# Kernel tuning notes

Measured on AMD Instinct MI355X. Metric: run time of the kernel, lower is better.

## Reference

```python
import jax, jax.numpy as jnp
import numpy as np

B, N_ROWS, N_COLS, CTRL = 16384, 2048, 128, 1024
EPS = 1e-16


def setup_inputs() -> dict:
    key = jax.random.key(0)
    k1, k2, k3 = jax.random.split(key, 3)
    x = jax.random.normal(k1, (B, CTRL), dtype=jnp.float32)
    W_fc = jax.random.normal(k2, (CTRL, N_COLS + 6), dtype=jnp.float32) * 0.02
    b_fc = jnp.zeros((N_COLS + 6,), dtype=jnp.float32)
    M = jax.random.normal(k3, (N_ROWS, N_COLS), dtype=jnp.float32)
    # initial weighting: softmax of bias with w_bias[0]=100 -> ~one-hot at row 0
    w_bias = jnp.zeros((N_ROWS,), dtype=jnp.float32).at[0].set(100.0)
    w_prev = jnp.broadcast_to(jax.nn.softmax(w_bias), (B, N_ROWS))
    return {"x": x, "W_fc": W_fc, "b_fc": b_fc, "M": M, "w_prev": w_prev}


def reference(x, W_fc, b_fc, M, w_prev):
    # dense projection + split
    h = x @ W_fc + b_fc                      # [B, N_COLS+6]
    k = h[:, :N_COLS]                        # [B, N_COLS]
    beta = jax.nn.softplus(h[:, N_COLS:N_COLS + 1])          # [B, 1]
    g = jax.nn.sigmoid(h[:, N_COLS + 1:N_COLS + 2])          # [B, 1]
    s = jax.nn.softmax(h[:, N_COLS + 2:N_COLS + 5], axis=-1) # [B, 3]
    gamma = 1.0 + jax.nn.softplus(h[:, N_COLS + 5:N_COLS + 6])  # [B, 1]

    # content addressing: cosine similarity against every memory row
    k_norm = jnp.linalg.norm(k, axis=-1, keepdims=True)       # [B, 1]
    M_norm = jnp.linalg.norm(M, axis=-1)                      # [N_ROWS]
    sim = (k @ M.T) / (k_norm * M_norm[None, :] + EPS)        # [B, N_ROWS]
    w_c = jax.nn.softmax(beta * sim, axis=-1)

    # interpolation gate
    w_g = g * w_c + (1.0 - g) * w_prev

    # circular shift convolution (shifts -1, 0, +1)
    w_tilde = (s[:, 0:1] * jnp.roll(w_g, 1, axis=1)
               + s[:, 1:2] * w_g
               + s[:, 2:3] * jnp.roll(w_g, -1, axis=1))

    # sharpening
    w_pow = (w_tilde + EPS) ** gamma
    w = w_pow / jnp.sum(w_pow, axis=-1, keepdims=True)

    # weighted read
    r = w @ M                                                 # [B, N_COLS]
    return r
```

## Files before the change

### kernel.cpp

```cpp
#include <hip/hip_runtime.h>
#include <hip/hip_bf16.h>

#define NB    16384
#define NR    2048
#define NC    128
#define KCTRL 1024
#define EPSF  1e-16f
#define ESTR  2056
#define XSTR  1032

typedef __attribute__((ext_vector_type(8))) short bf16x8;
typedef __attribute__((ext_vector_type(4))) float f32x4;

__device__ __forceinline__ float softplus_f(float x) {
    return fmaxf(x, 0.f) + log1pf(__expf(-fabsf(x)));
}
__device__ __forceinline__ unsigned short f2bf(float f) {
    __hip_bfloat16 h = __float2bfloat16(f);
    return *(unsigned short*)&h;
}
__device__ __forceinline__ float bf2f(unsigned short u) {
    __hip_bfloat16 h;
    *(unsigned short*)&h = u;
    return __bfloat162float(h);
}

__device__ __forceinline__ size_t swz(int n, int k, int nch) {
    return ((size_t)((n >> 4) * nch + (k >> 5)) * 64 + ((k >> 3) & 3) * 16 + (n & 15)) * 8 + (k & 7);
}

__global__ __launch_bounds__(64) void prep_all(const float* __restrict__ M,
                                               unsigned short* __restrict__ Mb_sw,
                                               unsigned short* __restrict__ Mt_sw,
                                               float* __restrict__ imn,
                                               const float* __restrict__ W,
                                               unsigned short* __restrict__ Wt_sw) {
    const int bid = blockIdx.x;
    const int l = threadIdx.x;
    if (bid < NR) {
        const int i = bid;
        const float v0 = M[(size_t)i * NC + l];
        const float v1 = M[(size_t)i * NC + 64 + l];
        Mb_sw[swz(i, l, 4)]      = f2bf(v0);
        Mb_sw[swz(i, 64 + l, 4)] = f2bf(v1);
        Mt_sw[swz(l, i, 64)]      = f2bf(v0);
        Mt_sw[swz(64 + l, i, 64)] = f2bf(v1);
        float s = v0 * v0 + v1 * v1;
        #pragma unroll
        for (int m = 1; m < 64; m <<= 1) s += __shfl_xor(s, m);
        if (l == 0) imn[i] = 1.f / sqrtf(s);
    } else {
        const int k = bid - NR;
        Wt_sw[swz(l, k, 32)]      = f2bf(W[(size_t)k * 134 + l]);
        Wt_sw[swz(64 + l, k, 32)] = f2bf(W[(size_t)k * 134 + 64 + l]);
        if (l < 6) {
            Wt_sw[swz(128 + l, k, 32)] = f2bf(W[(size_t)k * 134 + 128 + l]);
        }
    }
}

__global__ __launch_bounds__(512, 4) void fused_ntm(const float* __restrict__ x,
                                                    const unsigned short* __restrict__ Wt_sw,
                                                    const float* __restrict__ bfc,
                                                    const unsigned short* __restrict__ Mb_sw,
                                                    const unsigned short* __restrict__ Mt_sw,
                                                    const float* __restrict__ imn,
                                                    const float* __restrict__ wprev,
                                                    float* __restrict__ out) {
    __shared__ __align__(16) unsigned short E_s[16][ESTR];
    __shared__ __align__(16) unsigned short k_s[16][136];
    __shared__ float h6s[16][6];
    __shared__ float ksum[16];
    __shared__ float scal_s[16][6];
    __shared__ float wred[16][8];
    __shared__ float fa_s[16], fc_s[16], invZ_s[16];

    unsigned short (*x_s)[XSTR] = (unsigned short(*)[XSTR])E_s;

    const int tid  = threadIdx.x;
    const int w    = tid >> 6;
    const int lane = tid & 63;
    const int quad = lane >> 4;
    const int l16  = lane & 15;
    const int b0   = blockIdx.x * 16;

    if (tid < 16) ksum[tid] = 0.f;

    #pragma unroll
    for (int p = 0; p < 8; p++) {
        const int idx = p * 512 + tid;
        const int row = idx >> 8;
        const int c4  = idx & 255;
        const float4 v = *(const float4*)(x + (size_t)(b0 + row) * KCTRL + c4 * 4);
        unsigned short* d = &x_s[row][c4 * 4];
        d[0] = f2bf(v.x); d[1] = f2bf(v.y); d[2] = f2bf(v.z); d[3] = f2bf(v.w);
    }
    __syncthreads();

    {
        f32x4 accF = {0.f, 0.f, 0.f, 0.f};
        f32x4 accH = {0.f, 0.f, 0.f, 0.f};
        const unsigned short* wbp = Wt_sw + (size_t)w * 16384 + lane * 8;
        const unsigned short* whp = Wt_sw + (size_t)8 * 16384 + lane * 8;
        bf16x8 bc0 = *(const bf16x8*)(wbp);
        bf16x8 bc1 = *(const bf16x8*)(wbp + 512);
        #pragma unroll
        for (int i = 0; i < 32; i += 2) {
            bf16x8 bn0, bn1;
            if (i < 30) {
                bn0 = *(const bf16x8*)(wbp + (size_t)(i + 2) * 512);
                bn1 = *(const bf16x8*)(wbp + (size_t)(i + 3) * 512);
            }
            const bf16x8 a0 = *(const bf16x8*)&x_s[l16][i * 32 + quad * 8];
            const bf16x8 a1 = *(const bf16x8*)&x_s[l16][(i + 1) * 32 + quad * 8];
            accF = __builtin_amdgcn_mfma_f32_16x16x32_bf16(a0, bc0, accF, 0, 0, 0);
            accF = __builtin_amdgcn_mfma_f32_16x16x32_bf16(a1, bc1, accF, 0, 0, 0);
            if (w == 0) {
                const bf16x8 h0 = *(const bf16x8*)(whp + (size_t)i * 512);
                const bf16x8 h1 = *(const bf16x8*)(whp + (size_t)(i + 1) * 512);
                accH = __builtin_amdgcn_mfma_f32_16x16x32_bf16(a0, h0, accH, 0, 0, 0);
                accH = __builtin_amdgcn_mfma_f32_16x16x32_bf16(a1, h1, accH, 0, 0, 0);
            }
            bc0 = bn0; bc1 = bn1;
        }
        __syncthreads();

        const float bb = bfc[w * 16 + l16];
        float part[4];
        #pragma unroll
        for (int reg = 0; reg < 4; reg++) {
            const int m = quad * 4 + reg;
            const float v = accF[reg] + bb;
            k_s[m][w * 16 + l16] = f2bf(v);
            part[reg] = v * v;
        }
        #pragma unroll
        for (int s = 1; s < 16; s <<= 1) {
            #pragma unroll
            for (int reg = 0; reg < 4; reg++) part[reg] += __shfl_xor(part[reg], s);
        }
        if (l16 == 0) {
            #pragma unroll
            for (int reg = 0; reg < 4; reg++) atomicAdd(&ksum[quad * 4 + reg], part[reg]);
        }
        if (w == 0 && l16 < 6) {
            const float bh = bfc[128 + l16];
            #pragma unroll
            for (int reg = 0; reg < 4; reg++) h6s[quad * 4 + reg][l16] = accH[reg] + bh;
        }
    }
    __syncthreads();

    if (tid < 16) {
        const float kn = sqrtf(ksum[tid]);
        const float* h = h6s[tid];
        const float beta = softplus_f(h[0]);
        const float g = 1.f / (1.f + __expf(-h[1]));
        const float m3 = fmaxf(h[2], fmaxf(h[3], h[4]));
        const float e0 = __expf(h[2] - m3), e1 = __expf(h[3] - m3), e2 = __expf(h[4] - m3);
        const float inv = 1.f / (e0 + e1 + e2);
        scal_s[tid][0] = beta / kn;
        scal_s[tid][1] = g;
        scal_s[tid][2] = e0 * inv;
        scal_s[tid][3] = e1 * inv;
        scal_s[tid][4] = e2 * inv;
        scal_s[tid][5] = 1.f + softplus_f(h[5]);
    }
    __syncthreads();

    {
        float cbs[4];
        #pragma unroll
        for (int reg = 0; reg < 4; reg++) cbs[reg] = scal_s[quad * 4 + reg][0];

        const bf16x8 af0 = *(const bf16x8*)&k_s[l16][quad * 8];
        const bf16x8 af1 = *(const bf16x8*)&k_s[l16][32 + quad * 8];
        const bf16x8 af2 = *(const bf16x8*)&k_s[l16][64 + quad * 8];
        const bf16x8 af3 = *(const bf16x8*)&k_s[l16][96 + quad * 8];

        const unsigned short* bp0 = Mb_sw + (size_t)(w * 16) * 2048 + lane * 8;
        bf16x8 f0 = *(const bf16x8*)(bp0);
        bf16x8 f1 = *(const bf16x8*)(bp0 + 512);
        bf16x8 f2 = *(const bf16x8*)(bp0 + 1024);
        bf16x8 f3 = *(const bf16x8*)(bp0 + 1536);
        float imc = imn[w * 256 + l16];

        float Sp[4] = {0.f, 0.f, 0.f, 0.f};
        #pragma unroll
        for (int t = 0; t < 16; t++) {
            const int nt = w * 16 + t;
            bf16x8 g0, g1, g2, g3;
            float imnext = 0.f;
            if (t < 15) {
                const unsigned short* bp = Mb_sw + (size_t)(nt + 1) * 2048 + lane * 8;
                g0 = *(const bf16x8*)(bp);
                g1 = *(const bf16x8*)(bp + 512);
                g2 = *(const bf16x8*)(bp + 1024);
                g3 = *(const bf16x8*)(bp + 1536);
                imnext = imn[(nt + 1) * 16 + l16];
            }
            f32x4 aA = {0.f, 0.f, 0.f, 0.f};
            f32x4 aB = {0.f, 0.f, 0.f, 0.f};
            aA = __builtin_amdgcn_mfma_f32_16x16x32_bf16(af0, f0, aA, 0, 0, 0);
            aB = __builtin_amdgcn_mfma_f32_16x16x32_bf16(af2, f2, aB, 0, 0, 0);
            aA = __builtin_amdgcn_mfma_f32_16x16x32_bf16(af1, f1, aA, 0, 0, 0);
            aB = __builtin_amdgcn_mfma_f32_16x16x32_bf16(af3, f3, aB, 0, 0, 0);
            const int n0 = nt * 16;
            #pragma unroll
            for (int reg = 0; reg < 4; reg++) {
                const float e = __expf((aA[reg] + aB[reg]) * cbs[reg] * imc);
                E_s[quad * 4 + reg][n0 + l16] = f2bf(e);
                Sp[reg] += e;
            }
            f0 = g0; f1 = g1; f2 = g2; f3 = g3; imc = imnext;
        }
        #pragma unroll
        for (int s = 1; s < 16; s <<= 1) {
            #pragma unroll
            for (int reg = 0; reg < 4; reg++) Sp[reg] += __shfl_xor(Sp[reg], s);
        }
        if (l16 == 0) {
            #pragma unroll
            for (int reg = 0; reg < 4; reg++) wred[quad * 4 + reg][w] = Sp[reg];
        }
    }
    __syncthreads();
    if (tid < 16) {
        float S = 0.f;
        #pragma unroll
        for (int i = 0; i < 8; i++) S += wred[tid][i];
        const float g = scal_s[tid][1];
        fa_s[tid] = g / S;
        fc_s[tid] = 1.f - g;
    }
    __syncthreads();

    {
        const int row  = tid >> 5;
        const int g    = tid & 31;
        const int base = tid & 32;
        const float s0 = scal_s[row][2], s1 = scal_s[row][3], s2 = scal_s[row][4];
        const float gmm = scal_s[row][5];
        const float fa = fa_s[row], fcm = fc_s[row];
        const float* wp = wprev + (size_t)(b0 + row) * NR;

        int c0 = g * 8;
        bf16x8 E8c = *(const bf16x8*)&E_s[row][c0];
        float eLc  = bf2f(E_s[row][(c0 + NR - 1) & (NR - 1)]);
        float eRc  = bf2f(E_s[row][c0 + 8]);
        float4 wac = *(const float4*)(wp + c0);
        float4 wbc = *(const float4*)(wp + c0 + 4);
        float wpLc = wp[(c0 + NR - 1) & (NR - 1)];
        float wpRc = wp[c0 + 8];

        float Zp = 0.f, carry = 0.f, E0sav = 0.f;
        #pragma unroll
        for (int j = 0; j < 8; j++) {
            bf16x8 E8n; float eLn = 0.f, eRn = 0.f, wpLn = 0.f, wpRn = 0.f;
            float4 wan, wbn;
            if (j < 7) {
                const int c1 = c0 + 256;
                E8n  = *(const bf16x8*)&E_s[row][c1];
                eLn  = bf2f(E_s[row][c1 - 1]);
                eRn  = bf2f(E_s[row][(c1 + 8) & (NR - 1)]);
                wan  = *(const float4*)(wp + c1);
                wbn  = *(const float4*)(wp + c1 + 4);
                wpLn = wp[c1 - 1];
                wpRn = wp[(c1 + 8) & (NR - 1)];
            }
            float ef[8];
            #pragma unroll
            for (int i = 0; i < 8; i++) ef[i] = bf2f((unsigned short)E8c[i]);
            if (j == 0) E0sav = __shfl(ef[0], base);
            const float eL = (g == 0 && j > 0) ? carry : eLc;
            const float eR = (g == 31 && j == 7) ? E0sav : eRc;
            carry = __shfl(ef[7], base + 31);

            float wg[10];
            wg[0] = fmaf(fa, eL,    fcm * wpLc);
            wg[1] = fmaf(fa, ef[0], fcm * wac.x);
            wg[2] = fmaf(fa, ef[1], fcm * wac.y);
            wg[3] = fmaf(fa, ef[2], fcm * wac.z);
            wg[4] = fmaf(fa, ef[3], fcm * wac.w);
            wg[5] = fmaf(fa, ef[4], fcm * wbc.x);
            wg[6] = fmaf(fa, ef[5], fcm * wbc.y);
            wg[7] = fmaf(fa, ef[6], fcm * wbc.z);
            wg[8] = fmaf(fa, ef[7], fcm * wbc.w);
            wg[9] = fmaf(fa, eR,    fcm * wpRc);

            bf16x8 out8;
            #pragma unroll
            for (int i = 0; i < 8; i++) {
                const float wt = fmaf(s0, wg[i], fmaf(s1, wg[i + 1], s2 * wg[i + 2])) + EPSF;
                const float pw = exp2f(gmm * log2f(wt));
                Zp += pw;
                out8[i] = (short)f2bf(pw);
            }
            *(bf16x8*)&E_s[row][c0] = out8;

            c0 += 256;
            E8c = E8n; eLc = eLn; eRc = eRn;
            wac = wan; wbc = wbn; wpLc = wpLn; wpRc = wpRn;
        }
        #pragma unroll
        for (int s = 1; s < 32; s <<= 1) Zp += __shfl_xor(Zp, s);
        if (g == 0) invZ_s[row] = 1.f / Zp;
    }
    __syncthreads();

    {
        f32x4 acc0 = {0.f, 0.f, 0.f, 0.f};
        f32x4 acc1 = {0.f, 0.f, 0.f, 0.f};
        f32x4 acc2 = {0.f, 0.f, 0.f, 0.f};
        f32x4 acc3 = {0.f, 0.f, 0.f, 0.f};
        const unsigned short* bp = Mt_sw + (size_t)w * 32768 + lane * 8;
        bf16x8 c0v = *(const bf16x8*)(bp);
        bf16x8 c1v = *(const bf16x8*)(bp + 512);
        bf16x8 c2v = *(const bf16x8*)(bp + 1024);
        bf16x8 c3v = *(const bf16x8*)(bp + 1536);
        #pragma unroll
        for (int k0 = 0; k0 < NR; k0 += 128) {
            bf16x8 n0v, n1v, n2v, n3v;
            if (k0 < NR - 128) {
                const unsigned short* np = bp + (size_t)((k0 >> 5) + 4) * 512;
                n0v = *(const bf16x8*)(np);
                n1v = *(const bf16x8*)(np + 512);
                n2v = *(const bf16x8*)(np + 1024);
                n3v = *(const bf16x8*)(np + 1536);
            }
            const bf16x8 a0 = *(const bf16x8*)&E_s[l16][k0 + quad * 8];
            const bf16x8 a1 = *(const bf16x8*)&E_s[l16][k0 + 32 + quad * 8];
            const bf16x8 a2 = *(const bf16x8*)&E_s[l16][k0 + 64 + quad * 8];
            const bf16x8 a3 = *(const bf16x8*)&E_s[l16][k0 + 96 + quad * 8];
            acc0 = __builtin_amdgcn_mfma_f32_16x16x32_bf16(a0, c0v, acc0, 0, 0, 0);
            acc1 = __builtin_amdgcn_mfma_f32_16x16x32_bf16(a1, c1v, acc1, 0, 0, 0);
            acc2 = __builtin_amdgcn_mfma_f32_16x16x32_bf16(a2, c2v, acc2, 0, 0, 0);
            acc3 = __builtin_amdgcn_mfma_f32_16x16x32_bf16(a3, c3v, acc3, 0, 0, 0);
            c0v = n0v; c1v = n1v; c2v = n2v; c3v = n3v;
        }
        #pragma unroll
        for (int reg = 0; reg < 4; reg++) {
            const int m = quad * 4 + reg;
            const float v = (acc0[reg] + acc1[reg]) + (acc2[reg] + acc3[reg]);
            out[(size_t)(b0 + m) * NC + w * 16 + l16] = v * invZ_s[m];
        }
    }
}

extern "C" void kernel_launch(void* const* d_in, const int* in_sizes, int n_in,
                              void* d_out, int out_size, void* d_ws, size_t ws_size,
                              hipStream_t stream) {
    const float* x     = (const float*)d_in[0];
    const float* Wfc   = (const float*)d_in[1];
    const float* bfc   = (const float*)d_in[2];
    const float* M     = (const float*)d_in[3];
    const float* wprev = (const float*)d_in[4];
    float* out = (float*)d_out;

    char* ws = (char*)d_ws;
    float*          imn   = (float*)(ws);
    unsigned short* Mb_sw = (unsigned short*)(ws + 8192);
    unsigned short* Mt_sw = (unsigned short*)(ws + 532480);
    unsigned short* Wt_sw = (unsigned short*)(ws + 1056768);

    hipLaunchKernelGGL(prep_all, dim3(NR + KCTRL), dim3(64), 0, stream,
                       M, Mb_sw, Mt_sw, imn, Wfc, Wt_sw);
    hipLaunchKernelGGL(fused_ntm, dim3(NB / 16), dim3(512), 0, stream,
                       x, Wt_sw, bfc, Mb_sw, Mt_sw, imn, wprev, out);
}
```

Baseline: 292.0 us.

## Split the memory-row weighting into two halves to halve shared buffer and raise occupancy

The shared E buffer now holds only 1024 of the 2048 memory rows, and the kernel processes the rows in two halves. The second half's similarity exps are computed first for the softmax sum and then recomputed after the first half's read GEMM. Boundary values for the circular shift are saved in a small edge array, and the sharpening normaliser is accumulated across both halves. This roughly halves LDS use so launch bounds can go from 4 to 6 blocks per CU. The cost is a repeated second-half similarity GEMM plus exp, extra barriers, and the removal of the register prefetch of M tiles.

```diff
diff --git a/kernel.cpp b/kernel.cpp
--- a/kernel.cpp
+++ b/kernel.cpp
@@ -6,8 +6,8 @@
 #define NC    128
 #define KCTRL 1024
 #define EPSF  1e-16f
-#define ESTR  2056
-#define XSTR  1032
+#define NH    1024
+#define HSTR  1032
 
 typedef __attribute__((ext_vector_type(8))) short bf16x8;
 typedef __attribute__((ext_vector_type(4))) float f32x4;
@@ -24,6 +24,7 @@
     *(unsigned short*)&h = u;
     return __bfloat162float(h);
 }
+__device__ __forceinline__ float bfround(float f) { return bf2f(f2bf(f)); }
 
 __device__ __forceinline__ size_t swz(int n, int k, int nch) {
     return ((size_t)((n >> 4) * nch + (k >> 5)) * 64 + ((k >> 3) & 3) * 16 + (n & 15)) * 8 + (k & 7);
@@ -59,7 +60,7 @@
     }
 }
 
-__global__ __launch_bounds__(512, 4) void fused_ntm(const float* __restrict__ x,
+__global__ __launch_bounds__(512, 6) void fused_ntm(const float* __restrict__ x,
                                                     const unsigned short* __restrict__ Wt_sw,
                                                     const float* __restrict__ bfc,
                                                     const unsigned short* __restrict__ Mb_sw,
@@ -67,15 +68,15 @@
                                                     const float* __restrict__ imn,
                                                     const float* __restrict__ wprev,
                                                     float* __restrict__ out) {
-    __shared__ __align__(16) unsigned short E_s[16][ESTR];
+    __shared__ __align__(16) unsigned short E_s[16][HSTR];
     __shared__ __align__(16) unsigned short k_s[16][136];
     __shared__ float h6s[16][6];
     __shared__ float ksum[16];
     __shared__ float scal_s[16][6];
-    __shared__ float wred[16][8];
+    __shared__ float wred[16][16];
+    __shared__ float edge_s[16][4];
+    __shared__ float z0_s[16];
     __shared__ float fa_s[16], fc_s[16], invZ_s[16];
-
-    unsigned short (*x_s)[XSTR] = (unsigned short(*)[XSTR])E_s;
 
     const int tid  = threadIdx.x;
     const int w    = tid >> 6;
@@ -92,7 +93,7 @@
         const int row = idx >> 8;
         const int c4  = idx & 255;
         const float4 v = *(const float4*)(x + (size_t)(b0 + row) * KCTRL + c4 * 4);
-        unsigned short* d = &x_s[row][c4 * 4];
+        unsigned short* d = &E_s[row][c4 * 4];
         d[0] = f2bf(v.x); d[1] = f2bf(v.y); d[2] = f2bf(v.z); d[3] = f2bf(v.w);
     }
     __syncthreads();
@@ -111,8 +112,8 @@
                 bn0 = *(const bf16x8*)(wbp + (size_t)(i + 2) * 512);
                 bn1 = *(const bf16x8*)(wbp + (size_t)(i + 3) * 512);
             }
-            const bf16x8 a0 = *(const bf16x8*)&x_s[l16][i * 32 + quad * 8];
-            const bf16x8 a1 = *(const bf16x8*)&x_s[l16][(i + 1) * 32 + quad * 8];
+            const bf16x8 a0 = *(const bf16x8*)&E_s[l16][i * 32 + quad * 8];
+            const bf16x8 a1 = *(const bf16x8*)&E_s[l16][(i + 1) * 32 + quad * 8];
             accF = __builtin_amdgcn_mfma_f32_16x16x32_bf16(a0, bc0, accF, 0, 0, 0);
             accF = __builtin_amdgcn_mfma_f32_16x16x32_bf16(a1, bc1, accF, 0, 0, 0);
             if (w == 0) {
@@ -172,47 +173,79 @@
         float cbs[4];
         #pragma unroll
         for (int reg = 0; reg < 4; reg++) cbs[reg] = scal_s[quad * 4 + reg][0];
-
         const bf16x8 af0 = *(const bf16x8*)&k_s[l16][quad * 8];
         const bf16x8 af1 = *(const bf16x8*)&k_s[l16][32 + quad * 8];
         const bf16x8 af2 = *(const bf16x8*)&k_s[l16][64 + quad * 8];
         const bf16x8 af3 = *(const bf16x8*)&k_s[l16][96 + quad * 8];
 
-        const unsigned short* bp0 = Mb_sw + (size_t)(w * 16) * 2048 + lane * 8;
-        bf16x8 f0 = *(const bf16x8*)(bp0);
-        bf16x8 f1 = *(const bf16x8*)(bp0 + 512);
-        bf16x8 f2 = *(const bf16x8*)(bp0 + 1024);
-        bf16x8 f3 = *(const bf16x8*)(bp0 + 1536);
-        float imc = imn[w * 256 + l16];
-
         float Sp[4] = {0.f, 0.f, 0.f, 0.f};
         #pragma unroll
-        for (int t = 0; t < 16; t++) {
-            const int nt = w * 16 + t;
-            bf16x8 g0, g1, g2, g3;
-            float imnext = 0.f;
-            if (t < 15) {
-                const unsigned short* bp = Mb_sw + (size_t)(nt + 1) * 2048 + lane * 8;
-                g0 = *(const bf16x8*)(bp);
-                g1 = *(const bf16x8*)(bp + 512);
-                g2 = *(const bf16x8*)(bp + 1024);
-                g3 = *(const bf16x8*)(bp + 1536);
-                imnext = imn[(nt + 1) * 16 + l16];
-            }
+        for (int t = 0; t < 8; t++) {
+            const int nt = 64 + w * 8 + t;
+            const unsigned short* bp = Mb_sw + (size_t)nt * 2048 + lane * 8;
+            const bf16x8 m0 = *(const bf16x8*)(bp);
+            const bf16x8 m1 = *(const bf16x8*)(bp + 512);
+            const bf16x8 m2 = *(const bf16x8*)(bp + 1024);
+            const bf16x8 m3 = *(const bf16x8*)(bp + 1536);
+            const float imc = imn[nt * 16 + l16];
             f32x4 aA = {0.f, 0.f, 0.f, 0.f};
             f32x4 aB = {0.f, 0.f, 0.f, 0.f};
-            aA = __builtin_amdgcn_mfma_f32_16x16x32_bf16(af0, f0, aA, 0, 0, 0);
-            aB = __builtin_amdgcn_mfma_f32_16x16x32_bf16(af2, f2, aB, 0, 0, 0);
-            aA = __builtin_amdgcn_mfma_f32_16x16x32_bf16(af1, f1, aA, 0, 0, 0);
-            aB = __builtin_amdgcn_mfma_f32_16x16x32_bf16(af3, f3, aB, 0, 0, 0);
+            aA = __builtin_amdgcn_mfma_f32_16x16x32_bf16(af0, m0, aA, 0, 0, 0);
+            aB = __builtin_amdgcn_mfma_f32_16x16x32_bf16(af2, m2, aB, 0, 0, 0);
+            aA = __builtin_amdgcn_mfma_f32_16x16x32_bf16(af1, m1, aA, 0, 0, 0);
+            aB = __builtin_amdgcn_mfma_f32_16x16x32_bf16(af3, m3, aB, 0, 0, 0);
+            #pragma unroll
+            for (int reg = 0; reg < 4; reg++) {
+                const float e = __expf((aA[reg] + aB[reg]) * cbs[reg] * imc);
+                Sp[reg] += e;
+                if (nt == 64 && l16 == 0)  edge_s[quad * 4 + reg][2] = bfround(e);
+                if (nt == 127 && l16 == 15) edge_s[quad * 4 + reg][3] = bfround(e);
+            }
+        }
+        #pragma unroll
+        for (int s = 1; s < 16; s <<= 1) {
+            #pragma unroll
+            for (int reg = 0; reg < 4; reg++) Sp[reg] += __shfl_xor(Sp[reg], s);
+        }
+        if (l16 == 0) {
+            #pragma unroll
+            for (int reg = 0; reg < 4; reg++) wred[quad * 4 + reg][w] = Sp[reg];
+        }
+    }
+    {
+        float cbs[4];
+        #pragma unroll
+        for (int reg = 0; reg < 4; reg++) cbs[reg] = scal_s[quad * 4 + reg][0];
+        const bf16x8 af0 = *(const bf16x8*)&k_s[l16][quad * 8];
+        const bf16x8 af1 = *(const bf16x8*)&k_s[l16][32 + quad * 8];
+        const bf16x8 af2 = *(const bf16x8*)&k_s[l16][64 + quad * 8];
+        const bf16x8 af3 = *(const bf16x8*)&k_s[l16][96 + quad * 8];
+
+        float Sp[4] = {0.f, 0.f, 0.f, 0.f};
+        #pragma unroll
+        for (int t = 0; t < 8; t++) {
+            const int nt = w * 8 + t;
+            const unsigned short* bp = Mb_sw + (size_t)nt * 2048 + lane * 8;
+            const bf16x8 m0 = *(const bf16x8*)(bp);
+            const bf16x8 m1 = *(const bf16x8*)(bp + 512);
+            const bf16x8 m2 = *(const bf16x8*)(bp + 1024);
+            const bf16x8 m3 = *(const bf16x8*)(bp + 1536);
+            const float imc = imn[nt * 16 + l16];
+            f32x4 aA = {0.f, 0.f, 0.f, 0.f};
+            f32x4 aB = {0.f, 0.f, 0.f, 0.f};
+            aA = __builtin_amdgcn_mfma_f32_16x16x32_bf16(af0, m0, aA, 0, 0, 0);
+            aB = __builtin_amdgcn_mfma_f32_16x16x32_bf16(af2, m2, aB, 0, 0, 0);
+            aA = __builtin_amdgcn_mfma_f32_16x16x32_bf16(af1, m1, aA, 0, 0, 0);
+            aB = __builtin_amdgcn_mfma_f32_16x16x32_bf16(af3, m3, aB, 0, 0, 0);
             const int n0 = nt * 16;
             #pragma unroll
             for (int reg = 0; reg < 4; reg++) {
                 const float e = __expf((aA[reg] + aB[reg]) * cbs[reg] * imc);
                 E_s[quad * 4 + reg][n0 + l16] = f2bf(e);
                 Sp[reg] += e;
-            }
-            f0 = g0; f1 = g1; f2 = g2; f3 = g3; imc = imnext;
+                if (nt == 0 && l16 == 0)   edge_s[quad * 4 + reg][0] = bfround(e);
+                if (nt == 63 && l16 == 15) edge_s[quad * 4 + reg][1] = bfround(e);
+            }
         }
         #pragma unroll
         for (int s = 1; s < 16; s <<= 1) {
@@ -221,48 +254,51 @@
         }
         if (l16 == 0) {
             #pragma unroll
-            for (int reg = 0; reg < 4; reg++) wred[quad * 4 + reg][w] = Sp[reg];
+            for (int reg = 0; reg < 4; reg++) wred[quad * 4 + reg][8 + w] = Sp[reg];
         }
     }
     __syncthreads();
     if (tid < 16) {
         float S = 0.f;
         #pragma unroll
-        for (int i = 0; i < 8; i++) S += wred[tid][i];
+        for (int i = 0; i < 16; i++) S += wred[tid][i];
         const float g = scal_s[tid][1];
         fa_s[tid] = g / S;
         fc_s[tid] = 1.f - g;
     }
     __syncthreads();
 
+    const int prow  = tid >> 5;
+    const int pg    = tid & 31;
+    const int pbase = tid & 32;
+    const float* wp = wprev + (size_t)(b0 + prow) * NR;
+
     {
-        const int row  = tid >> 5;
-        const int g    = tid & 31;
-        const int base = tid & 32;
-        const float s0 = scal_s[row][2], s1 = scal_s[row][3], s2 = scal_s[row][4];
-        const float gmm = scal_s[row][5];
-        const float fa = fa_s[row], fcm = fc_s[row];
-        const float* wp = wprev + (size_t)(b0 + row) * NR;
-
-        int c0 = g * 8;
-        bf16x8 E8c = *(const bf16x8*)&E_s[row][c0];
-        float eLc  = bf2f(E_s[row][(c0 + NR - 1) & (NR - 1)]);
-        float eRc  = bf2f(E_s[row][c0 + 8]);
+        const float s0 = scal_s[prow][2], s1 = scal_s[prow][3], s2 = scal_s[prow][4];
+        const float gmm = scal_s[prow][5];
+        const float fa = fa_s[prow], fcm = fc_s[prow];
+        const float eWL = edge_s[prow][3];
+        const float eWR = edge_s[prow][2];
+
+        int c0 = pg * 8;
+        bf16x8 E8c = *(const bf16x8*)&E_s[prow][c0];
+        float eLc  = bf2f(E_s[prow][(c0 + NH - 1) & (NH - 1)]);
+        float eRc  = bf2f(E_s[prow][c0 + 8]);
         float4 wac = *(const float4*)(wp + c0);
         float4 wbc = *(const float4*)(wp + c0 + 4);
         float wpLc = wp[(c0 + NR - 1) & (NR - 1)];
-        float wpRc = wp[c0 + 8];
-
-        float Zp = 0.f, carry = 0.f, E0sav = 0.f;
-        #pragma unroll
-        for (int j = 0; j < 8; j++) {
+        float wpRc = wp[(c0 + 8) & (NR - 1)];
+
+        float Zp = 0.f, carry = 0.f;
+        #pragma unroll
+        for (int j = 0; j < 4; j++) {
             bf16x8 E8n; float eLn = 0.f, eRn = 0.f, wpLn = 0.f, wpRn = 0.f;
             float4 wan, wbn;
-            if (j < 7) {
+            if (j < 3) {
                 const int c1 = c0 + 256;
-                E8n  = *(const bf16x8*)&E_s[row][c1];
-                eLn  = bf2f(E_s[row][c1 - 1]);
-                eRn  = bf2f(E_s[row][(c1 + 8) & (NR - 1)]);
+                E8n  = *(const bf16x8*)&E_s[prow][c1];
+                eLn  = bf2f(E_s[prow][c1 - 1]);
+                eRn  = bf2f(E_s[prow][c1 + 8]);
                 wan  = *(const float4*)(wp + c1);
                 wbn  = *(const float4*)(wp + c1 + 4);
                 wpLn = wp[c1 - 1];
@@ -271,10 +307,9 @@
             float ef[8];
             #pragma unroll
             for (int i = 0; i < 8; i++) ef[i] = bf2f((unsigned short)E8c[i]);
-            if (j == 0) E0sav = __shfl(ef[0], base);
-            const float eL = (g == 0 && j > 0) ? carry : eLc;
-            const float eR = (g == 31 && j == 7) ? E0sav : eRc;
-            carry = __shfl(ef[7], base + 31);
+            const float eL = (pg == 0) ? ((j == 0) ? eWL : carry) : eLc;
+            const float eR = (pg == 31 && j == 3) ? eWR : eRc;
+            carry = __shfl(ef[7], pbase + 31);
 
             float wg[10];
             wg[0] = fmaf(fa, eL,    fcm * wpLc);
@@ -296,7 +331,7 @@
                 Zp += pw;
                 out8[i] = (short)f2bf(pw);
             }
-            *(bf16x8*)&E_s[row][c0] = out8;
+            *(bf16x8*)&E_s[prow][c0] = out8;
 
             c0 += 256;
             E8c = E8n; eLc = eLn; eRc = eRn;
@@ -304,46 +339,157 @@
         }
         #pragma unroll
         for (int s = 1; s < 32; s <<= 1) Zp += __shfl_xor(Zp, s);
-        if (g == 0) invZ_s[row] = 1.f / Zp;
+        if (pg == 0) z0_s[prow] = Zp;
+    }
+    __syncthreads();
+
+    f32x4 acc0 = {0.f, 0.f, 0.f, 0.f};
+    f32x4 acc1 = {0.f, 0.f, 0.f, 0.f};
+    f32x4 acc2 = {0.f, 0.f, 0.f, 0.f};
+    f32x4 acc3 = {0.f, 0.f, 0.f, 0.f};
+    const unsigned short* bp2 = Mt_sw + (size_t)w * 32768 + lane * 8;
+    #pragma unroll
+    for (int k0 = 0; k0 < NH; k0 += 128) {
+        const unsigned short* cp = bp2 + (size_t)(k0 >> 5) * 512;
+        const bf16x8 c0v = *(const bf16x8*)(cp);
+        const bf16x8 c1v = *(const bf16x8*)(cp + 512);
+        const bf16x8 c2v = *(const bf16x8*)(cp + 1024);
+        const bf16x8 c3v = *(const bf16x8*)(cp + 1536);
+        const bf16x8 a0 = *(const bf16x8*)&E_s[l16][k0 + quad * 8];
+        const bf16x8 a1 = *(const bf16x8*)&E_s[l16][k0 + 32 + quad * 8];
+        const bf16x8 a2 = *(const bf16x8*)&E_s[l16][k0 + 64 + quad * 8];
+        const bf16x8 a3 = *(const bf16x8*)&E_s[l16][k0 + 96 + quad * 8];
+        acc0 = __builtin_amdgcn_mfma_f32_16x16x32_bf16(a0, c0v, acc0, 0, 0, 0);
+        acc1 = __builtin_amdgcn_mfma_f32_16x16x32_bf16(a1, c1v, acc1, 0, 0, 0);
+        acc2 = __builtin_amdgcn_mfma_f32_16x16x32_bf16(a2, c2v, acc2, 0, 0, 0);
+        acc3 = __builtin_amdgcn_mfma_f32_16x16x32_bf16(a3, c3v, acc3, 0, 0, 0);
     }
     __syncthreads();
 
     {
-        f32x4 acc0 = {0.f, 0.f, 0.f, 0.f};
-        f32x4 acc1 = {0.f, 0.f, 0.f, 0.f};
-        f32x4 acc2 = {0.f, 0.f, 0.f, 0.f};
-        f32x4 acc3 = {0.f, 0.f, 0.f, 0.f};
-        const unsigned short* bp = Mt_sw + (size_t)w * 32768 + lane * 8;
-        bf16x8 c0v = *(const bf16x8*)(bp);
-        bf16x8 c1v = *(const bf16x8*)(bp + 512);
-        bf16x8 c2v = *(const bf16x8*)(bp + 1024);
-        bf16x8 c3v = *(const bf16x8*)(bp + 1536);
-        #pragma unroll
-        for (int k0 = 0; k0 < NR; k0 += 128) {
-            bf16x8 n0v, n1v, n2v, n3v;
-            if (k0 < NR - 128) {
-                const unsigned short* np = bp + (size_t)((k0 >> 5) + 4) * 512;
-                n0v = *(const bf16x8*)(np);
-                n1v = *(const bf16x8*)(np + 512);
-                n2v = *(const bf16x8*)(np + 1024);
-                n3v = *(const bf16x8*)(np + 1536);
-            }
-            const bf16x8 a0 = *(const bf16x8*)&E_s[l16][k0 + quad * 8];
-            const bf16x8 a1 = *(const bf16x8*)&E_s[l16][k0 + 32 + quad * 8];
-            const bf16x8 a2 = *(const bf16x8*)&E_s[l16][k0 + 64 + quad * 8];
-            const bf16x8 a3 = *(const bf16x8*)&E_s[l16][k0 + 96 + quad * 8];
-            acc0 = __builtin_amdgcn_mfma_f32_16x16x32_bf16(a0, c0v, acc0, 0, 0, 0);
-            acc1 = __builtin_amdgcn_mfma_f32_16x16x32_bf16(a1, c1v, acc1, 0, 0, 0);
-            acc2 = __builtin_amdgcn_mfma_f32_16x16x32_bf16(a2, c2v, acc2, 0, 0, 0);
-            acc3 = __builtin_amdgcn_mfma_f32_16x16x32_bf16(a3, c3v, acc3, 0, 0, 0);
-            c0v = n0v; c1v = n1v; c2v = n2v; c3v = n3v;
-        }
-        #pragma unroll
-        for (int reg = 0; reg < 4; reg++) {
-            const int m = quad * 4 + reg;
-            const float v = (acc0[reg] + acc1[reg]) + (acc2[reg] + acc3[reg]);
-            out[(size_t)(b0 + m) * NC + w * 16 + l16] = v * invZ_s[m];
-        }
+        float cbs[4];
+        #pragma unroll
+        for (int reg = 0; reg < 4; reg++) cbs[reg] = scal_s[quad * 4 + reg][0];
+        const bf16x8 af0 = *(const bf16x8*)&k_s[l16][quad * 8];
+        const bf16x8 af1 = *(const bf16x8*)&k_s[l16][32 + quad * 8];
+        const bf16x8 af2 = *(const bf16x8*)&k_s[l16][64 + quad * 8];
+        const bf16x8 af3 = *(const bf16x8*)&k_s[l16][96 + quad * 8];
+        #pragma unroll
+        for (int t = 0; t < 8; t++) {
+            const int nt = 64 + w * 8 + t;
+            const unsigned short* bp = Mb_sw + (size_t)nt * 2048 + lane * 8;
+            const bf16x8 m0 = *(const bf16x8*)(bp);
+            const bf16x8 m1 = *(const bf16x8*)(bp + 512);
+            const bf16x8 m2 = *(const bf16x8*)(bp + 1024);
+            const bf16x8 m3 = *(const bf16x8*)(bp + 1536);
+            const float imc = imn[nt * 16 + l16];
+            f32x4 aA = {0.f, 0.f, 0.f, 0.f};
+            f32x4 aB = {0.f, 0.f, 0.f, 0.f};
+            aA = __builtin_amdgcn_mfma_f32_16x16x32_bf16(af0, m0, aA, 0, 0, 0);
+            aB = __builtin_amdgcn_mfma_f32_16x16x32_bf16(af2, m2, aB, 0, 0, 0);
+            aA = __builtin_amdgcn_mfma_f32_16x16x32_bf16(af1, m1, aA, 0, 0, 0);
+            aB = __builtin_amdgcn_mfma_f32_16x16x32_bf16(af3, m3, aB, 0, 0, 0);
+            const int n0 = (nt - 64) * 16;
+            #pragma unroll
+            for (int reg = 0; reg < 4; reg++) {
+                const float e = __expf((aA[reg] + aB[reg]) * cbs[reg] * imc);
+                E_s[quad * 4 + reg][n0 + l16] = f2bf(e);
+            }
+        }
+    }
+    __syncthreads();
+
+    {
+        const float s0 = scal_s[prow][2], s1 = scal_s[prow][3], s2 = scal_s[prow][4];
+        const float gmm = scal_s[prow][5];
+        const float fa = fa_s[prow], fcm = fc_s[prow];
+        const float eWL = edge_s[prow][1];
+        const float eWR = edge_s[prow][0];
+
+        int c0 = pg * 8;
+        bf16x8 E8c = *(const bf16x8*)&E_s[prow][c0];
+        float eLc  = bf2f(E_s[prow][(c0 + NH - 1) & (NH - 1)]);
+        float eRc  = bf2f(E_s[prow][c0 + 8]);
+        float4 wac = *(const float4*)(wp + NH + c0);
+        float4 wbc = *(const float4*)(wp + NH + c0 + 4);
+        float wpLc = wp[(NH + c0 + NR - 1) & (NR - 1)];
+        float wpRc = wp[(NH + c0 + 8) & (NR - 1)];
+
+        float Zp = 0.f, carry = 0.f;
+        #pragma unroll
+        for (int j = 0; j < 4; j++) {
+            bf16x8 E8n; float eLn = 0.f, eRn = 0.f, wpLn = 0.f, wpRn = 0.f;
+            float4 wan, wbn;
+            if (j < 3) {
+                const int c1 = c0 + 256;
+                E8n  = *(const bf16x8*)&E_s[prow][c1];
+                eLn  = bf2f(E_s[prow][c1 - 1]);
+                eRn  = bf2f(E_s[prow][c1 + 8]);
+                wan  = *(const float4*)(wp + NH + c1);
+                wbn  = *(const float4*)(wp + NH + c1 + 4);
+                wpLn = wp[NH + c1 - 1];
+                wpRn = wp[(NH + c1 + 8) & (NR - 1)];
+            }
+            float ef[8];
+            #pragma unroll
+            for (int i = 0; i < 8; i++) ef[i] = bf2f((unsigned short)E8c[i]);
+            const float eL = (pg == 0) ? ((j == 0) ? eWL : carry) : eLc;
+            const float eR = (pg == 31 && j == 3) ? eWR : eRc;
+            carry = __shfl(ef[7], pbase + 31);
+
+            float wg[10];
+            wg[0] = fmaf(fa, eL,    fcm * wpLc);
+            wg[1] = fmaf(fa, ef[0], fcm * wac.x);
+            wg[2] = fmaf(fa, ef[1], fcm * wac.y);
+            wg[3] = fmaf(fa, ef[2], fcm * wac.z);
+            wg[4] = fmaf(fa, ef[3], fcm * wac.w);
+            wg[5] = fmaf(fa, ef[4], fcm * wbc.x);
+            wg[6] = fmaf(fa, ef[5], fcm * wbc.y);
+            wg[7] = fmaf(fa, ef[6], fcm * wbc.z);
+            wg[8] = fmaf(fa, ef[7], fcm * wbc.w);
+            wg[9] = fmaf(fa, eR,    fcm * wpRc);
+
+            bf16x8 out8;
+            #pragma unroll
+            for (int i = 0; i < 8; i++) {
+                const float wt = fmaf(s0, wg[i], fmaf(s1, wg[i + 1], s2 * wg[i + 2])) + EPSF;
+                const float pw = exp2f(gmm * log2f(wt));
+                Zp += pw;
+                out8[i] = (short)f2bf(pw);
+            }
+            *(bf16x8*)&E_s[prow][c0] = out8;
+
+            c0 += 256;
+            E8c = E8n; eLc = eLn; eRc = eRn;
+            wac = wan; wbc = wbn; wpLc = wpLn; wpRc = wpRn;
+        }
+        #pragma unroll
+        for (int s = 1; s < 32; s <<= 1) Zp += __shfl_xor(Zp, s);
+        if (pg == 0) invZ_s[prow] = 1.f / (z0_s[prow] + Zp);
+    }
+    __syncthreads();
+
+    #pragma unroll
+    for (int k0 = 0; k0 < NH; k0 += 128) {
+        const unsigned short* cp = bp2 + (size_t)(32 + (k0 >> 5)) * 512;
+        const bf16x8 c0v = *(const bf16x8*)(cp);
+        const bf16x8 c1v = *(const bf16x8*)(cp + 512);
+        const bf16x8 c2v = *(const bf16x8*)(cp + 1024);
+        const bf16x8 c3v = *(const bf16x8*)(cp + 1536);
+        const bf16x8 a0 = *(const bf16x8*)&E_s[l16][k0 + quad * 8];
+        const bf16x8 a1 = *(const bf16x8*)&E_s[l16][k0 + 32 + quad * 8];
+        const bf16x8 a2 = *(const bf16x8*)&E_s[l16][k0 + 64 + quad * 8];
+        const bf16x8 a3 = *(const bf16x8*)&E_s[l16][k0 + 96 + quad * 8];
+        acc0 = __builtin_amdgcn_mfma_f32_16x16x32_bf16(a0, c0v, acc0, 0, 0, 0);
+        acc1 = __builtin_amdgcn_mfma_f32_16x16x32_bf16(a1, c1v, acc1, 0, 0, 0);
+        acc2 = __builtin_amdgcn_mfma_f32_16x16x32_bf16(a2, c2v, acc2, 0, 0, 0);
+        acc3 = __builtin_amdgcn_mfma_f32_16x16x32_bf16(a3, c3v, acc3, 0, 0, 0);
+    }
+    #pragma unroll
+    for (int reg = 0; reg < 4; reg++) {
+        const int m = quad * 4 + reg;
+        const float v = (acc0[reg] + acc1[reg]) + (acc2[reg] + acc3[reg]);
+        out[(size_t)(b0 + m) * NC + w * 16 + l16] = v * invZ_s[m];
     }
 }
 
```

After: 500.4 us. 71.4% more time.
